# Kernel optimization log

Measured on AMD Instinct MI355X. Metric: run time of the kernel, lower is better.

Reference implementation:

```python
import jax, jax.numpy as jnp
import numpy as np

K = 11            # filter_size
SPAN = K // 2
BLUR = 4
NUM_ITER = 5      # default num_iter of GaussCRF.forward
UNARY_WEIGHT = 1.0


def avg_pool(x, b):
    # count_include_pad=False avg_pool2d; H,W divisible by b so no padding needed
    B, C, H, W = x.shape
    return x.reshape(B, C, H // b, b, W // b, b).mean(axis=(3, 5))


def extract_patches(x):
    # [B,C,H,W] -> [B,C,K*K,H,W]; patch index i*K+j <-> shift (i-SPAN, j-SPAN), zero padded
    # (matches F.unfold(x, K, 1, SPAN) reshaped to [B,C,K,K,H,W])
    B, C, H, W = x.shape
    xp = jnp.pad(x, ((0, 0), (0, 0), (SPAN, SPAN), (SPAN, SPAN)))
    cols = [xp[:, :, i:i + H, j:j + W] for i in range(K) for j in range(K)]
    return jnp.stack(cols, axis=2)


def shift_mask(H, W, dtype):
    # valid[ij, x, y] = 1 where the shifted pixel (x+dx, y+dy) is in-bounds
    d = jnp.arange(K) - SPAN
    ax = jnp.arange(H)[None, :] + d[:, None]   # [K,H]
    ay = jnp.arange(W)[None, :] + d[:, None]   # [K,W]
    mx = (ax >= 0) & (ax < H)
    my = (ay >= 0) & (ay < W)
    m = mx[:, None, :, None] & my[None, :, None, :]   # [K,K,H,W]
    return m.reshape(K * K, H, W).astype(dtype)


def gauss_kernel(feats):
    # feats: [B,Cf,h,w] (already blurred) -> [B,K*K,h,w]
    # g[b, ij, x, y] = exp(-0.5 * sum_c (f[x+dx,y+dy] - f[x,y])^2), zero where out-of-bounds
    B, C, H, W = feats.shape
    cols = extract_patches(feats)                      # [B,C,K*K,h,w]
    diff2 = (cols - feats[:, :, None]) ** 2
    g = jnp.exp(-0.5 * diff2.sum(axis=1))              # [B,K*K,h,w]
    return g * shift_mask(H, W, feats.dtype)[None]


def reference(unary, img, pos_sdims, col_schan, pos_compat, col_compat, weight):
    B, C, H, W = unary.shape
    dt = unary.dtype

    # pairwise features (mesh is a deterministic buffer)
    mesh = jnp.stack(jnp.meshgrid(jnp.arange(H, dtype=dt), jnp.arange(W, dtype=dt), indexing='ij'))  # [2,H,W]
    pos_feats = jnp.broadcast_to(mesh[None] * pos_sdims, (B, 2, H, W))
    col_feats = img * col_schan                        # use_bias=False

    # merged Gaussian kernel at blurred resolution (merge=True, norm='none')
    g = (pos_compat * gauss_kernel(avg_pool(pos_feats, BLUR))
         + col_compat * gauss_kernel(avg_pool(col_feats, BLUR)))   # [B,K*K,h,w]

    lg_unary = jax.nn.log_softmax(unary, axis=1)       # logsoftmax=True
    pred = lg_unary
    for it in range(NUM_ITER):
        p = avg_pool(pred, BLUR)                       # [B,C,h,w]
        cols = extract_patches(p)                      # [B,C,K*K,h,w]
        msg = jnp.einsum('bkxy,bckxy->bcxy', g, cols)  # local-window message passing
        msg = jax.image.resize(msg, (B, C, H, W), method='bilinear')  # align_corners=False
        pred = (UNARY_WEIGHT - weight) * lg_unary + weight * msg
        if it != NUM_ITER - 1:                         # final_softmax=False
            pred = jax.nn.softmax(pred, axis=1)
    return pred


def setup_inputs() -> dict:
    key = jax.random.key(0)
    k1, k2 = jax.random.split(key)
    B, C, H, W = 2, 21, 512, 512
    return {
        'unary': jax.random.normal(k1, (B, C, H, W), jnp.float32),
        'img': jax.random.uniform(k2, (B, 3, H, W), jnp.float32) * 255.0,  # 0..255 image range (schan=1/13)
        'pos_sdims': jnp.array([1.0 / 3.0], jnp.float32),
        'col_schan': jnp.array([1.0 / 13.0], jnp.float32),
        'pos_compat': jnp.array([3.0], jnp.float32),
        'col_compat': jnp.array([10.0], jnp.float32),
        'weight': jnp.array([0.2], jnp.float32),
    }
```

## Files before the change

kernel.cpp:

```cpp
#include <hip/hip_runtime.h>
#include <cmath>


#define BB 2
#define CC 21
#define HH 512
#define WW 512
#define HP 128
#define WP 128
#define KF 11
#define SPAN 5
#define NB 121
#define NITER 5
#define PLF (HH*WW)
#define PLP (HP*WP)
#define PC 24
#define PSTR2 12
#define RSTR2 13
#define PT2_N (18*18*PSTR2)

__global__ __launch_bounds__(256) void prep_k(const float* __restrict__ img,
                                              const float* __restrict__ col_schan,
                                              const float* __restrict__ unary,
                                              float* __restrict__ cf,
                                              float* __restrict__ p) {
    int bid = blockIdx.x;
    int t = threadIdx.x;
    if (bid >= 1024) {
        int idx = (bid - 1024)*256 + t;
        int Y  = idx & (WP-1);
        int X  = (idx >> 7) & (HP-1);
        int bc = idx >> 14;
        const float* base = img + ((size_t)bc*HH + X*4)*WW + Y*4;
        float s = 0.f;
        #pragma unroll
        for (int i = 0; i < 4; ++i)
            #pragma unroll
            for (int j = 0; j < 4; ++j)
                s += base[i*WW + j];
        cf[idx] = s * (1.f/16.f) * col_schan[0];
        return;
    }
    int b = bid >> 9, rem = bid & 511, tx = rem >> 4, ty = rem & 15;
    int row = t >> 4, c2 = t & 15;
    int x = tx*16 + row, y = ty*32 + 2*c2;
    size_t base = (size_t)b*CC*PLF + (size_t)x*WW + y;
    float va[CC], vb[CC];
    float ma = -1e30f, mb = -1e30f;
    #pragma unroll
    for (int c = 0; c < CC; ++c) {
        float2 u = *(const float2*)(unary + base + (size_t)c*PLF);
        va[c] = u.x; vb[c] = u.y;
        ma = fmaxf(ma, u.x); mb = fmaxf(mb, u.y);
    }
    float sa = 0.f, sb = 0.f;
    #pragma unroll
    for (int c = 0; c < CC; ++c) { sa += expf(va[c]-ma); sb += expf(vb[c]-mb); }
    float lsa = ma + logf(sa), lsb = mb + logf(sb);
    float out[PC];
    #pragma unroll
    for (int c = 0; c < PC; ++c) out[c] = 0.f;
    #pragma unroll
    for (int c = 0; c < CC; ++c) {
        float sm = (va[c]-lsa) + (vb[c]-lsb);
        sm += __shfl_xor(sm, 1);
        sm += __shfl_xor(sm, 16);
        sm += __shfl_xor(sm, 32);
        out[c] = sm * (1.f/16.f);
    }
    int lane = t & 63;
    if ((lane & 49) == 0) {
        int X = tx*4 + (t >> 6), Y = ty*8 + (c2 >> 1);
        float4* dst = (float4*)(p + ((size_t)(b*HP + X)*WP + Y)*PC);
        const float4* src = (const float4*)out;
        dst[0]=src[0]; dst[1]=src[1]; dst[2]=src[2];
        dst[3]=src[3]; dst[4]=src[4]; dst[5]=src[5];
    }
}

__global__ void gauss_k(const float* __restrict__ cf,
                        const float* __restrict__ pos_sdims,
                        const float* __restrict__ pos_compat,
                        const float* __restrict__ col_compat,
                        float* __restrict__ g) {
    int tile = blockIdx.y;
    int e = blockIdx.x * blockDim.x + threadIdx.x;
    if (e >= NB*64) return;
    int pos = e & 63;
    int ij  = e >> 6;
    int tY = tile & 15, tX = (tile >> 4) & 15, b = tile >> 8;
    int X = tX*8 + (pos >> 3), Y = tY*8 + (pos & 7);
    int di = ij / KF - SPAN;
    int dj = ij % KF - SPAN;
    int Xn = X + di, Yn = Y + dj;
    float val = 0.f;
    if (Xn >= 0 && Xn < HP && Yn >= 0 && Yn < WP) {
        const float* cb = cf + (size_t)b*3*PLP;
        int o0 = X*WP + Y, o = Xn*WP + Yn;
        float d0 = cb[o]         - cb[o0];
        float d1 = cb[PLP + o]   - cb[PLP + o0];
        float d2 = cb[2*PLP + o] - cb[2*PLP + o0];
        float cd2 = d0*d0 + d1*d1 + d2*d2;
        float ps  = 4.f * pos_sdims[0];
        float pd2 = ps*ps * (float)(di*di + dj*dj);
        val = pos_compat[0] * expf(-0.5f*pd2) + col_compat[0] * expf(-0.5f*cd2);
    }
    g[(size_t)tile*NB*64 + e] = val;
}

__global__ __launch_bounds__(256) void msg_k(const float* __restrict__ g,
                                             const float* __restrict__ p,
                                             float* __restrict__ msg) {
    int zz = blockIdx.z, tx = blockIdx.y, ty = blockIdx.x;
    int b = zz >> 1, half = zz & 1;
    int koff = half*3, coff = half*12;
    int t = threadIdx.x;
    __shared__ __align__(16) float sh[PT2_N];
    float* pt = sh;
    int X0 = tx*8 - SPAN, Y0 = ty*8 - SPAN;
    const float4* pg = (const float4*)(p + (size_t)b*PLP*PC);
    for (int e = t; e < 18*18*3; e += 256) {
        int pos = e / 3, k = e % 3;
        int r = pos / 18, cl = pos % 18;
        int gX = X0 + r, gY = Y0 + cl;
        float4 v = {0.f,0.f,0.f,0.f};
        if (gX >= 0 && gX < HP && gY >= 0 && gY < WP)
            v = pg[(size_t)(gX*WP + gY)*6 + k + koff];
        *(float4*)(pt + pos*PSTR2 + k*4) = v;
    }
    __syncthreads();
    int w = t >> 6, lane = t & 63;
    int x = lane >> 3, y = lane & 7;
    const float* gt = g + (size_t)((b*16 + tx)*16 + ty)*NB*64 + lane;
    int d0 = w*3, d1 = (w == 3) ? KF : w*3 + 3;
    float acc[12];
    #pragma unroll
    for (int c = 0; c < 12; ++c) acc[c] = 0.f;
    for (int di = d0; di < d1; ++di) {
        const float* prow = pt + ((x+di)*18 + y)*PSTR2;
        const float* grow = gt + (size_t)(di*KF)*64;
        #pragma unroll
        for (int dj = 0; dj < KF; ++dj) {
            float gv = grow[(size_t)dj*64];
            const float4* sp = (const float4*)(prow + dj*PSTR2);
            float4 q0 = sp[0], q1 = sp[1], q2 = sp[2];
            acc[0]  = fmaf(gv, q0.x, acc[0]);  acc[1]  = fmaf(gv, q0.y, acc[1]);
            acc[2]  = fmaf(gv, q0.z, acc[2]);  acc[3]  = fmaf(gv, q0.w, acc[3]);
            acc[4]  = fmaf(gv, q1.x, acc[4]);  acc[5]  = fmaf(gv, q1.y, acc[5]);
            acc[6]  = fmaf(gv, q1.z, acc[6]);  acc[7]  = fmaf(gv, q1.w, acc[7]);
            acc[8]  = fmaf(gv, q2.x, acc[8]);  acc[9]  = fmaf(gv, q2.y, acc[9]);
            acc[10] = fmaf(gv, q2.z, acc[10]); acc[11] = fmaf(gv, q2.w, acc[11]);
        }
    }
    __syncthreads();
    float* rb = sh;
    if (w > 0) {
        #pragma unroll
        for (int c = 0; c < 12; ++c) rb[((w-1)*64 + lane)*RSTR2 + c] = acc[c];
    }
    __syncthreads();
    if (w == 0) {
        int Xg = tx*8 + x, Yg = ty*8 + y;
        float* mb = msg + (size_t)b*CC*PLP + (size_t)Xg*WP + Yg;
        int nst = half ? 9 : 12;
        for (int c = 0; c < nst; ++c) {
            float s = ((acc[c] + rb[(0*64 + lane)*RSTR2 + c])
                              + rb[(1*64 + lane)*RSTR2 + c])
                              + rb[(2*64 + lane)*RSTR2 + c];
            mb[(size_t)(coff + c)*PLP] = s;
        }
    }
}

__global__ __launch_bounds__(256) void combine_k(const float* __restrict__ msg,
                                                 const float* __restrict__ unary,
                                                 const float* __restrict__ weight,
                                                 float* __restrict__ pnew,
                                                 float* __restrict__ pred,
                                                 int last) {
    int b = blockIdx.z, tx = blockIdx.y, ty = blockIdx.x;
    int t = threadIdx.x;
    __shared__ float ms[CC][6][10];
    const float* mb = msg + (size_t)b*CC*PLP;
    for (int e = t; e < CC*60; e += 256) {
        int c = e / 60, rr = (e / 10) % 6, cl = e % 10;
        int gX = tx*4 - 1 + rr; gX = gX < 0 ? 0 : (gX > HP-1 ? HP-1 : gX);
        int gY = ty*8 - 1 + cl; gY = gY < 0 ? 0 : (gY > WP-1 ? WP-1 : gY);
        ms[c][rr][cl] = mb[(size_t)c*PLP + gX*WP + gY];
    }
    __syncthreads();
    int row = t >> 4, c2 = t & 15;
    int x = tx*16 + row, y = ty*32 + 2*c2;
    size_t base = (size_t)b*CC*PLF + (size_t)x*WW + y;
    int rs = row & 3, q = row >> 2;
    float fx = (rs == 0) ? 0.625f : (rs == 1) ? 0.875f : (rs == 2) ? 0.125f : 0.375f;
    int i0 = q + (rs >> 1);
    int cs0 = (2*c2) & 3;
    int qc  = (2*c2) >> 2;
    float fya = (cs0 == 0) ? 0.625f : 0.125f;
    float fyb = (cs0 == 0) ? 0.875f : 0.375f;
    int j0 = qc + (cs0 >> 1);
    float gx0 = 1.f - fx;
    float wt = weight[0], uw = 1.f - wt;
    float va[CC], vb[CC];
    float ma = -1e30f, mbx = -1e30f;
    #pragma unroll
    for (int c = 0; c < CC; ++c) {
        float2 u = *(const float2*)(unary + base + (size_t)c*PLF);
        va[c] = u.x; vb[c] = u.y;
        ma = fmaxf(ma, u.x); mbx = fmaxf(mbx, u.y);
    }
    float sa = 0.f, sb = 0.f;
    #pragma unroll
    for (int c = 0; c < CC; ++c) { sa += expf(va[c]-ma); sb += expf(vb[c]-mbx); }
    float lsa = ma + logf(sa), lsb = mbx + logf(sb);
    #pragma unroll
    for (int c = 0; c < CC; ++c) {
        float m00 = ms[c][i0][j0],   m01 = ms[c][i0][j0+1];
        float m10 = ms[c][i0+1][j0], m11 = ms[c][i0+1][j0+1];
        float ca = gx0*m00 + fx*m10;
        float cb = gx0*m01 + fx*m11;
        float mua = (1.f-fya)*ca + fya*cb;
        float mub = (1.f-fyb)*ca + fyb*cb;
        va[c] = uw*(va[c]-lsa) + wt*mua;
        vb[c] = uw*(vb[c]-lsb) + wt*mub;
    }
    if (last) {
        #pragma unroll
        for (int c = 0; c < CC; ++c) {
            float2 o; o.x = va[c]; o.y = vb[c];
            *(float2*)(pred + base + (size_t)c*PLF) = o;
        }
    } else {
        float mma = -1e30f, mmb = -1e30f;
        #pragma unroll
        for (int c = 0; c < CC; ++c) { mma = fmaxf(mma, va[c]); mmb = fmaxf(mmb, vb[c]); }
        float ssa = 0.f, ssb = 0.f;
        #pragma unroll
        for (int c = 0; c < CC; ++c) {
            va[c] = expf(va[c]-mma); ssa += va[c];
            vb[c] = expf(vb[c]-mmb); ssb += vb[c];
        }
        float ia = 1.f/ssa, ib = 1.f/ssb;
        float out[PC];
        #pragma unroll
        for (int c = 0; c < PC; ++c) out[c] = 0.f;
        #pragma unroll
        for (int c = 0; c < CC; ++c) {
            float sm = va[c]*ia + vb[c]*ib;
            sm += __shfl_xor(sm, 1);
            sm += __shfl_xor(sm, 16);
            sm += __shfl_xor(sm, 32);
            out[c] = sm * (1.f/16.f);
        }
        int lane = t & 63;
        if ((lane & 49) == 0) {
            int X = tx*4 + (t >> 6), Y = ty*8 + (c2 >> 1);
            float4* dst = (float4*)(pnew + ((size_t)(b*HP + X)*WP + Y)*PC);
            const float4* src = (const float4*)out;
            dst[0]=src[0]; dst[1]=src[1]; dst[2]=src[2];
            dst[3]=src[3]; dst[4]=src[4]; dst[5]=src[5];
        }
    }
}

extern "C" void kernel_launch(void* const* d_in, const int* in_sizes, int n_in,
                              void* d_out, int out_size, void* d_ws, size_t ws_size,
                              hipStream_t stream) {
    const float* unary      = (const float*)d_in[0];
    const float* img        = (const float*)d_in[1];
    const float* pos_sdims  = (const float*)d_in[2];
    const float* col_schan  = (const float*)d_in[3];
    const float* pos_compat = (const float*)d_in[4];
    const float* col_compat = (const float*)d_in[5];
    const float* weight     = (const float*)d_in[6];
    float* pred = (float*)d_out;
    float* ws   = (float*)d_ws;

    size_t o = 0;
    float* cf  = ws + o;  o += (size_t)BB*3*PLP;
    float* g   = ws + o;  o += (size_t)BB*NB*PLP;
    float* msg = ws + o;  o += (size_t)BB*CC*PLP;
    float* pA  = ws + o;  o += (size_t)BB*PLP*PC;
    float* pB  = ws + o;
    float* pbuf[2] = {pA, pB};

    const int TB = 256;
    hipLaunchKernelGGL(prep_k, dim3(1408), dim3(TB), 0, stream,
                       img, col_schan, unary, cf, pA);
    hipLaunchKernelGGL(gauss_k, dim3((NB*64+TB-1)/TB, 512), dim3(TB), 0, stream,
                       cf, pos_sdims, pos_compat, col_compat, g);
    for (int it = 0; it < NITER; ++it) {
        hipLaunchKernelGGL(msg_k, dim3(16, 16, BB*2), dim3(256), 0, stream,
                           g, pbuf[it & 1], msg);
        hipLaunchKernelGGL(combine_k, dim3(16, 32, BB), dim3(256), 0, stream,
                           msg, unary, weight, pbuf[(it + 1) & 1],
                           pred, (it == NITER-1) ? 1 : 0);
    }
}
```

Before: 262.1 us.

## Fuse Gaussian kernel computation into message-passing kernel, drop g buffer

Removes the separate gauss_k launch and the global g buffer (B*121*128*128 floats). Each msg_k thread instead computes its 33 Gaussian weights in registers from the colour features, right before the local-window accumulation. This trades global reads of g on every iteration for recomputing the exps five times, once per iteration and per channel-half block. It also adds register pressure, with launch_bounds now set to 4 blocks per CU.

```diff
diff --git a/kernel.cpp b/kernel.cpp
--- a/kernel.cpp
+++ b/kernel.cpp
@@ -78,44 +78,53 @@
     }
 }
 
-__global__ void gauss_k(const float* __restrict__ cf,
-                        const float* __restrict__ pos_sdims,
-                        const float* __restrict__ pos_compat,
-                        const float* __restrict__ col_compat,
-                        float* __restrict__ g) {
-    int tile = blockIdx.y;
-    int e = blockIdx.x * blockDim.x + threadIdx.x;
-    if (e >= NB*64) return;
-    int pos = e & 63;
-    int ij  = e >> 6;
-    int tY = tile & 15, tX = (tile >> 4) & 15, b = tile >> 8;
-    int X = tX*8 + (pos >> 3), Y = tY*8 + (pos & 7);
-    int di = ij / KF - SPAN;
-    int dj = ij % KF - SPAN;
-    int Xn = X + di, Yn = Y + dj;
-    float val = 0.f;
-    if (Xn >= 0 && Xn < HP && Yn >= 0 && Yn < WP) {
-        const float* cb = cf + (size_t)b*3*PLP;
-        int o0 = X*WP + Y, o = Xn*WP + Yn;
-        float d0 = cb[o]         - cb[o0];
-        float d1 = cb[PLP + o]   - cb[PLP + o0];
-        float d2 = cb[2*PLP + o] - cb[2*PLP + o0];
-        float cd2 = d0*d0 + d1*d1 + d2*d2;
-        float ps  = 4.f * pos_sdims[0];
-        float pd2 = ps*ps * (float)(di*di + dj*dj);
-        val = pos_compat[0] * expf(-0.5f*pd2) + col_compat[0] * expf(-0.5f*cd2);
-    }
-    g[(size_t)tile*NB*64 + e] = val;
-}
-
-__global__ __launch_bounds__(256) void msg_k(const float* __restrict__ g,
-                                             const float* __restrict__ p,
-                                             float* __restrict__ msg) {
+__global__ __launch_bounds__(256, 4) void msg_k(const float* __restrict__ cf,
+                                                const float* __restrict__ p,
+                                                const float* __restrict__ pos_sdims,
+                                                const float* __restrict__ pos_compat,
+                                                const float* __restrict__ col_compat,
+                                                float* __restrict__ msg) {
     int zz = blockIdx.z, tx = blockIdx.y, ty = blockIdx.x;
     int b = zz >> 1, half = zz & 1;
     int koff = half*3, coff = half*12;
     int t = threadIdx.x;
     __shared__ __align__(16) float sh[PT2_N];
+    int w = t >> 6, lane = t & 63;
+    int x = lane >> 3, y = lane & 7;
+
+    const int rows[3] = {w*3, w*3 + 1, (w == 3) ? 10 : w*3 + 2};
+    const float gmsk2 = (w == 3) ? 0.f : 1.f;
+    float gvals[3][KF];
+    {
+        const int X = tx*8 + x, Y = ty*8 + y;
+        const float* cb = cf + (size_t)b*3*PLP;
+        const int o0 = X*WP + Y;
+        const float c0 = cb[o0], c1 = cb[PLP + o0], c2v = cb[2*PLP + o0];
+        const float ps  = 4.f * pos_sdims[0];
+        const float pcm = pos_compat[0], ccm = col_compat[0];
+        #pragma unroll
+        for (int r = 0; r < 3; ++r) {
+            const int di = rows[r] - SPAN;
+            const float rm = (r == 2) ? gmsk2 : 1.f;
+            #pragma unroll
+            for (int dj = 0; dj < KF; ++dj) {
+                const int djs = dj - SPAN;
+                int Xn = tx*8 + x + di, Yn = ty*8 + y + djs;
+                float val = 0.f;
+                if (Xn >= 0 && Xn < HP && Yn >= 0 && Yn < WP) {
+                    int o = Xn*WP + Yn;
+                    float d0 = cb[o]         - c0;
+                    float d1 = cb[PLP + o]   - c1;
+                    float d2 = cb[2*PLP + o] - c2v;
+                    float cd2 = d0*d0 + d1*d1 + d2*d2;
+                    float pd2 = ps*ps * (float)(di*di + djs*djs);
+                    val = pcm * expf(-0.5f*pd2) + ccm * expf(-0.5f*cd2);
+                }
+                gvals[r][dj] = val * rm;
+            }
+        }
+    }
+
     float* pt = sh;
     int X0 = tx*8 - SPAN, Y0 = ty*8 - SPAN;
     const float4* pg = (const float4*)(p + (size_t)b*PLP*PC);
@@ -129,19 +138,16 @@
         *(float4*)(pt + pos*PSTR2 + k*4) = v;
     }
     __syncthreads();
-    int w = t >> 6, lane = t & 63;
-    int x = lane >> 3, y = lane & 7;
-    const float* gt = g + (size_t)((b*16 + tx)*16 + ty)*NB*64 + lane;
-    int d0 = w*3, d1 = (w == 3) ? KF : w*3 + 3;
+
     float acc[12];
     #pragma unroll
     for (int c = 0; c < 12; ++c) acc[c] = 0.f;
-    for (int di = d0; di < d1; ++di) {
-        const float* prow = pt + ((x+di)*18 + y)*PSTR2;
-        const float* grow = gt + (size_t)(di*KF)*64;
+    #pragma unroll
+    for (int r = 0; r < 3; ++r) {
+        const float* prow = pt + ((x + rows[r])*18 + y)*PSTR2;
         #pragma unroll
         for (int dj = 0; dj < KF; ++dj) {
-            float gv = grow[(size_t)dj*64];
+            float gv = gvals[r][dj];
             const float4* sp = (const float4*)(prow + dj*PSTR2);
             float4 q0 = sp[0], q1 = sp[1], q2 = sp[2];
             acc[0]  = fmaf(gv, q0.x, acc[0]);  acc[1]  = fmaf(gv, q0.y, acc[1]);
@@ -279,7 +285,6 @@
 
     size_t o = 0;
     float* cf  = ws + o;  o += (size_t)BB*3*PLP;
-    float* g   = ws + o;  o += (size_t)BB*NB*PLP;
     float* msg = ws + o;  o += (size_t)BB*CC*PLP;
     float* pA  = ws + o;  o += (size_t)BB*PLP*PC;
     float* pB  = ws + o;
@@ -288,11 +293,10 @@
     const int TB = 256;
     hipLaunchKernelGGL(prep_k, dim3(1408), dim3(TB), 0, stream,
                        img, col_schan, unary, cf, pA);
-    hipLaunchKernelGGL(gauss_k, dim3((NB*64+TB-1)/TB, 512), dim3(TB), 0, stream,
-                       cf, pos_sdims, pos_compat, col_compat, g);
     for (int it = 0; it < NITER; ++it) {
         hipLaunchKernelGGL(msg_k, dim3(16, 16, BB*2), dim3(256), 0, stream,
-                           g, pbuf[it & 1], msg);
+                           cf, pbuf[it & 1], pos_sdims, pos_compat,
+                           col_compat, msg);
         hipLaunchKernelGGL(combine_k, dim3(16, 32, BB), dim3(256), 0, stream,
                            msg, unary, weight, pbuf[(it + 1) & 1],
                            pred, (it == NITER-1) ? 1 : 0);
```

After: 282.0 us. 7.6% more time.
